# Optimization experiments

Measured on AMD Instinct MI355X. Metric: run time of the kernel, lower is better.

## Reference

```python
import jax, jax.numpy as jnp
import numpy as np
import math

NUM_SOLU, BS, GS, ED, NH = 10, 32, 1000, 128, 8
KD = ED // NH
MSH = 16
NEG = -9e15


def setup_inputs() -> dict:
    key = jax.random.key(0)
    ks = jax.random.split(key, 16)
    node_embed = jax.random.normal(ks[0], (BS, GS, ED), jnp.float32)
    # random TSP tours: permutations per (solution, batch) -> each node a source exactly once
    solutions = jnp.argsort(jax.random.uniform(ks[1], (NUM_SOLU, BS, GS)), axis=-1).astype(jnp.int32)
    costs = jax.random.uniform(ks[2], (NUM_SOLU, BS), minval=1.0, maxval=2.0)  # positive tour costs
    dist = jax.random.uniform(ks[3], (BS, GS, GS), jnp.float32)
    solution_embed_old = jax.random.normal(ks[4], (BS, GS, ED), jnp.float32)
    s = 1.0 / math.sqrt(ED)
    Wq = jax.random.uniform(ks[5], (ED, ED), minval=-s, maxval=s)
    Wk = jax.random.uniform(ks[6], (ED, ED), minval=-s, maxval=s)
    m1 = math.sqrt(0.5)
    m2 = math.sqrt(1.0 / 16.0)
    mix1_weight = jax.random.uniform(ks[7], (NH, 2, MSH), minval=-m1, maxval=m1)
    mix1_bias = jax.random.uniform(ks[8], (NH, MSH), minval=-m1, maxval=m1)
    mix2_weight = jax.random.uniform(ks[9], (NH, MSH, 1), minval=-m2, maxval=m2)
    mix2_bias = jax.random.uniform(ks[10], (NH, 1), minval=-m2, maxval=m2)
    sh = 1.0 / math.sqrt(NH)
    norm_head_w = jax.random.uniform(ks[11], (NH,), minval=-sh, maxval=sh)
    sg = 1.0 / math.sqrt(ED)
    gru_w_ih = jax.random.uniform(ks[12], (3 * ED, ED), minval=-sg, maxval=sg)
    gru_w_hh = jax.random.uniform(ks[13], (3 * ED, ED), minval=-sg, maxval=sg)
    gru_b_ih = jax.random.uniform(ks[14], (3 * ED,), minval=-sg, maxval=sg)
    gru_b_hh = jax.random.uniform(ks[15], (3 * ED,), minval=-sg, maxval=sg)
    return dict(node_embed=node_embed, solutions=solutions, costs=costs, dist=dist,
                solution_embed_old=solution_embed_old, Wq=Wq, Wk=Wk,
                mix1_weight=mix1_weight, mix1_bias=mix1_bias,
                mix2_weight=mix2_weight, mix2_bias=mix2_bias,
                norm_head_w=norm_head_w, gru_w_ih=gru_w_ih, gru_w_hh=gru_w_hh,
                gru_b_ih=gru_b_ih, gru_b_hh=gru_b_hh)


def _forward(node_embed, costs, dist, solution_embed_old, Wq, Wk,
             mix1_weight, mix1_bias, mix2_weight, mix2_bias, norm_head_w,
             gru_w_ih, gru_w_hh, gru_b_ih, gru_b_hh, solutions):
    norm_factor = 1.0 / math.sqrt(KD)
    sqrt_qkv = KD ** 0.5
    nxt = jnp.roll(solutions, -1, axis=-1)                      # [S,B,T] successor in tour
    b_idx = jnp.arange(BS)[None, :, None]
    emb_solu = node_embed[b_idx, solutions]                     # [S,B,T,E] gather
    emb_next = node_embed[b_idx, nxt]                           # [S,B,T,E]
    q = (emb_solu @ Wq.T).reshape(NUM_SOLU, BS, GS, NH, KD)
    k = (emb_next @ Wk.T).reshape(NUM_SOLU, BS, GS, NH, KD)
    dot = jnp.einsum('sbthd,sbthd->sbth', q, k) * (norm_factor / sqrt_qkv)
    edge_cost = dist[b_idx, solutions, nxt]                     # [S,B,T]
    two = jnp.stack([dot, jnp.broadcast_to(edge_cost[..., None], dot.shape)], -1)  # [S,B,T,H,2]
    ms1 = jax.nn.relu(jnp.einsum('sbthe,hem->sbthm', two, mix1_weight) + mix1_bias)
    ms2 = jnp.einsum('sbthm,hmo->sbtho', ms1, mix2_weight)[..., 0] + mix2_bias[:, 0]  # [S,B,T,H]
    e = jnp.einsum('sbth,h->sbt', ms2, norm_head_w)             # norm_head Linear(n_heads,1)
    cost = e / costs[:, :, None]                                # [S,B,T]
    # scatter-add edge scores into dense [B,G,G] attention (tours = permutations,
    # so each (b, src) appears once per solution -> add == per-solution set + sum)
    bb = jnp.broadcast_to(b_idx, solutions.shape)
    attn = jnp.zeros((BS, GS, GS), node_embed.dtype).at[
        bb.reshape(-1), solutions.reshape(-1), nxt.reshape(-1)].add(cost.reshape(-1))
    attn = jnp.where(attn != 0.0, attn, NEG)
    ar = jnp.arange(GS)
    attn = attn.at[:, ar, ar].set(NEG)
    attn = jax.nn.softmax(attn, axis=-1)
    solu_embed = attn @ node_embed                              # [B,G,E]
    # torch GRUCell: gates order r,z,n
    x = solu_embed.reshape(-1, ED)
    h = solution_embed_old.reshape(-1, ED)
    gi = x @ gru_w_ih.T + gru_b_ih
    gh = h @ gru_w_hh.T + gru_b_hh
    i_r, i_z, i_n = jnp.split(gi, 3, axis=-1)
    h_r, h_z, h_n = jnp.split(gh, 3, axis=-1)
    r = jax.nn.sigmoid(i_r + h_r)
    z = jax.nn.sigmoid(i_z + h_z)
    n = jnp.tanh(i_n + r * h_n)
    new = ((1.0 - z) * n + z * h).reshape(BS, GS, ED)
    return jnp.stack([jax.nn.elu(new), new])                    # [2,B,G,E]


def reference(node_embed, solutions, costs, dist, solution_embed_old, Wq, Wk,
              mix1_weight, mix1_bias, mix2_weight, mix2_bias, norm_head_w,
              gru_w_ih, gru_w_hh, gru_b_ih, gru_b_hh):
    out = _forward(node_embed, costs, dist, solution_embed_old, Wq, Wk,
                   mix1_weight, mix1_bias, mix2_weight, mix2_bias, norm_head_w,
                   gru_w_ih, gru_w_hh, gru_b_ih, gru_b_hh, solutions)
    return (out[0], out[1])
```

## Files before the change

kernel.cpp:

```cpp
#include <hip/hip_runtime.h>
#include <math.h>

#define NS 10
#define NB 32
#define NG 1000
#define NE 128
#define NH 8
#define MSH 16

typedef __bf16 bf16x8 __attribute__((ext_vector_type(8)));
typedef float f32x4 __attribute__((ext_vector_type(4)));
typedef unsigned short ushort;
typedef ushort us8 __attribute__((ext_vector_type(8)));

__device__ __forceinline__ ushort f2bf(float f) {
    union { float f; unsigned u; } c; c.f = f;
    unsigned r = c.u + 0x7FFFu + ((c.u >> 16) & 1u);
    return (ushort)(r >> 16);
}
__device__ __forceinline__ float bflo(unsigned u) {
    union { unsigned v; float f; } c; c.v = u << 16; return c.f;
}
__device__ __forceinline__ float bfhi(unsigned u) {
    union { unsigned v; float f; } c; c.v = u & 0xFFFF0000u; return c.f;
}

__global__ __launch_bounds__(512) void qk_prep(
        const float* __restrict__ ne,
        const int* __restrict__ sol, const float* __restrict__ dist,
        const float* __restrict__ Wq, const float* __restrict__ Wk,
        const float* __restrict__ wih, const float* __restrict__ whh,
        float* __restrict__ QKf, ushort* __restrict__ ne_b,
        int* __restrict__ succ, float* __restrict__ edge_val,
        ushort* __restrict__ wih_b, ushort* __restrict__ whh_b) {
    const int tid = threadIdx.x;
    if (blockIdx.x >= 1000) {
        const int bid2 = blockIdx.x - 1000;
        if (bid2 < 625) {
            const int gidx = bid2 * 512 + tid;
            const int sb = gidx / NG;
            const int t = gidx - sb * NG;
            const int* srow = sol + (size_t)sb * NG;
            const int src = srow[t];
            const int tn = (t + 1 == NG) ? 0 : t + 1;
            const int dst = srow[tn];
            const int b = sb & 31;
            succ[(size_t)sb * NG + src] = dst;
            edge_val[(size_t)sb * NG + src] = dist[(size_t)(b * NG + src) * NG + dst];
        } else {
            const int wt = (bid2 - 625) * 512 + tid;
            const int e = wt * 8;
            const float* src = (e < 49152) ? wih : whh;
            ushort* dst = (e < 49152) ? wih_b : whh_b;
            const int off = (e < 49152) ? e : e - 49152;
            const float4 f0 = ((const float4*)(src + off))[0];
            const float4 f1 = ((const float4*)(src + off))[1];
            us8 v;
            v[0] = f2bf(f0.x); v[1] = f2bf(f0.y); v[2] = f2bf(f0.z); v[3] = f2bf(f0.w);
            v[4] = f2bf(f1.x); v[5] = f2bf(f1.y); v[6] = f2bf(f1.z); v[7] = f2bf(f1.w);
            *(us8*)(dst + off) = v;
        }
        return;
    }

    __shared__ __align__(16) ushort A[32 * 128];
    const int rowbase = blockIdx.x * 32;
    {
        const int r = tid >> 4, kc = tid & 15;
        const float4* s4 = (const float4*)(ne + (size_t)(rowbase + r) * NE);
        const float4 f0 = s4[kc * 2], f1 = s4[kc * 2 + 1];
        us8 v;
        v[0] = f2bf(f0.x); v[1] = f2bf(f0.y); v[2] = f2bf(f0.z); v[3] = f2bf(f0.w);
        v[4] = f2bf(f1.x); v[5] = f2bf(f1.y); v[6] = f2bf(f1.z); v[7] = f2bf(f1.w);
        *(us8*)&A[(r * 16 + (kc ^ (r & 7))) * 8] = v;
        *(us8*)&ne_b[(size_t)(rowbase + r) * NE + kc * 8] = v;
    }
    __syncthreads();

    const int w = tid >> 6, l = tid & 63;
    const int lr = l & 15, lg = l >> 4;

    f32x4 acc[2][2] = {};
#pragma unroll
    for (int ks = 0; ks < 4; ++ks) {
        bf16x8 a[2], b[2];
#pragma unroll
        for (int mf = 0; mf < 2; ++mf) {
            const int r = mf * 16 + lr;
            a[mf] = *(const bf16x8*)&A[(r * 16 + ((ks * 4 + lg) ^ (r & 7))) * 8];
        }
#pragma unroll
        for (int nf = 0; nf < 2; ++nf) {
            const int j = w * 32 + nf * 16 + lr;
            const float* Wrow = (j < 128) ? (Wq + (size_t)j * 128 + ks * 32 + lg * 8)
                                          : (Wk + (size_t)(j - 128) * 128 + ks * 32 + lg * 8);
            const float4 wf0 = ((const float4*)Wrow)[0];
            const float4 wf1 = ((const float4*)Wrow)[1];
            union { us8 u; bf16x8 bv; } cv;
            cv.u[0] = f2bf(wf0.x); cv.u[1] = f2bf(wf0.y); cv.u[2] = f2bf(wf0.z); cv.u[3] = f2bf(wf0.w);
            cv.u[4] = f2bf(wf1.x); cv.u[5] = f2bf(wf1.y); cv.u[6] = f2bf(wf1.z); cv.u[7] = f2bf(wf1.w);
            b[nf] = cv.bv;
        }
#pragma unroll
        for (int mf = 0; mf < 2; ++mf)
#pragma unroll
            for (int nf = 0; nf < 2; ++nf)
                acc[mf][nf] = __builtin_amdgcn_mfma_f32_16x16x32_bf16(a[mf], b[nf], acc[mf][nf], 0, 0, 0);
    }
#pragma unroll
    for (int mf = 0; mf < 2; ++mf)
#pragma unroll
        for (int nf = 0; nf < 2; ++nf)
#pragma unroll
            for (int q = 0; q < 4; ++q) {
                const int row = rowbase + mf * 16 + lg * 4 + q;
                const int col = w * 32 + nf * 16 + lr;
                if (w < 4)
                    QKf[(size_t)row * 192 + col] = acc[mf][nf][q];
                else
                    ((ushort*)(QKf + (size_t)row * 192 + 128))[col - 128] = f2bf(acc[mf][nf][q]);
            }
}

__global__ __launch_bounds__(256) void score_agg(
        const int* __restrict__ succ, const float* __restrict__ costs,
        const float* __restrict__ edge_val, const float* __restrict__ QKf,
        const ushort* __restrict__ ne_b,
        const float* __restrict__ m1w, const float* __restrict__ m1b,
        const float* __restrict__ m2w, const float* __restrict__ m2b,
        const float* __restrict__ nhw,
        unsigned* __restrict__ solu_b) {
    __shared__ float w1t[2][MSH][NH];
    __shared__ float b1t[MSH][NH];
    __shared__ float w2t[MSH][NH];
    __shared__ float b2s[NH];
    __shared__ float nws[NH];
    const int tid = threadIdx.x;
    {
        const int h = tid >> 5, e = (tid >> 4) & 1, m = tid & 15;
        w1t[e][m][h] = m1w[tid];
        if (tid < 128) {
            const int h2 = tid >> 4, m2 = tid & 15;
            b1t[m2][h2] = m1b[tid];
            w2t[m2][h2] = m2w[tid];
        }
        if (tid < NH) { b2s[tid] = m2b[tid]; nws[tid] = nhw[tid]; }
    }
    __syncthreads();

    const int bid = blockIdx.x;
    const int xcd = bid & 7;
    const int idx = bid >> 3;
    const int b = xcd + 8 * (idx / 250);
    const int g = (idx % 250) * 4 + (tid >> 6);
    const int lane = tid & 63;
    const int w = b * NG + g;
    const int h = lane & 7;
    const int sg = lane >> 3;

    int dstp[2]; float edgep[2];
    {
        const size_t o0 = (size_t)(sg * NB + b) * NG + g;
        const size_t o1 = (size_t)((8 + sg) * NB + b) * NG + g;
        dstp[0] = succ[o0];
        dstp[1] = (sg < 2) ? succ[o1] : 0;
        edgep[0] = edge_val[o0];
        edgep[1] = (sg < 2) ? edge_val[o1] : 0.f;
    }

    int d[NS];
#pragma unroll
    for (int s = 0; s < 8; ++s) d[s] = __shfl(dstp[0], s * 8);
    d[8] = __shfl(dstp[1], 0); d[9] = __shfl(dstp[1], 8);

    unsigned urow[NS];
#pragma unroll
    for (int s = 0; s < NS; ++s)
        urow[s] = ((const unsigned*)(ne_b + (size_t)(b * NG + d[s]) * NE))[lane];

    const float4* Qf = (const float4*)(QKf + (size_t)w * 192) + h * 4;
    const float4 qa = Qf[0], qb = Qf[1], qc = Qf[2], qd = Qf[3];
    uint4 k0p[2], k1p[2];
#pragma unroll
    for (int pass = 0; pass < 2; ++pass) {
        const uint4* Kr = (const uint4*)(QKf + (size_t)(b * NG + dstp[pass]) * 192 + 128);
        k0p[pass] = Kr[h * 2]; k1p[pass] = Kr[h * 2 + 1];
    }

    float val_p[2];
#pragma unroll
    for (int pass = 0; pass < 2; ++pass) {
        const uint4 k0 = k0p[pass], k1 = k1p[pass];
        float dd = qa.x * bflo(k0.x) + qa.y * bfhi(k0.x)
                 + qa.z * bflo(k0.y) + qa.w * bfhi(k0.y)
                 + qb.x * bflo(k0.z) + qb.y * bfhi(k0.z)
                 + qb.z * bflo(k0.w) + qb.w * bfhi(k0.w)
                 + qc.x * bflo(k1.x) + qc.y * bfhi(k1.x)
                 + qc.z * bflo(k1.y) + qc.w * bfhi(k1.y)
                 + qd.x * bflo(k1.z) + qd.y * bfhi(k1.z)
                 + qd.z * bflo(k1.w) + qd.w * bfhi(k1.w);
        dd *= 0.0625f;
        float ms2 = b2s[h];
#pragma unroll
        for (int m = 0; m < MSH; ++m) {
            float t = dd * w1t[0][m][h] + edgep[pass] * w1t[1][m][h] + b1t[m][h];
            t = fmaxf(t, 0.f);
            ms2 += t * w2t[m][h];
        }
        float contrib = ms2 * nws[h];
        contrib += __shfl_xor(contrib, 1);
        contrib += __shfl_xor(contrib, 2);
        contrib += __shfl_xor(contrib, 4);
        val_p[pass] = contrib;
    }

    const float va = __shfl(val_p[0], (lane & 7) * 8);
    const float vb = __shfl(val_p[1], (lane & 1) * 8);
    const int   da = __shfl(dstp[0], (lane & 7) * 8);
    const int   db = __shfl(dstp[1], (lane & 1) * 8);
    float v_own = (lane < 8) ? va : vb;
    const int d_own = (lane < 8) ? da : db;
    const int cidx = (lane < NS) ? lane : 0;
    v_own *= __builtin_amdgcn_rcpf(costs[cidx * NB + b]);

    float acc = v_own;
    bool first = true;
#pragma unroll
    for (int p = 0; p < NS; ++p) {
        const int   d_p = __shfl(d_own, p);
        const float v_p = __shfl(v_own, p);
        const bool eq = (d_p == d_own);
        first = first && (!eq || p >= lane);
        acc += (eq && p > lane) ? v_p : 0.f;
    }
    const bool surv = (lane < NS) && first && (acc != 0.f);

    float mval = surv ? acc : -3.0e38f;
    mval = fmaxf(mval, __shfl_xor(mval, 1));
    mval = fmaxf(mval, __shfl_xor(mval, 2));
    mval = fmaxf(mval, __shfl_xor(mval, 4));
    mval = fmaxf(mval, __shfl_xor(mval, 8));
    const float e = surv ? __expf(acc - mval) : 0.f;
    float den = e;
    den += __shfl_xor(den, 1);
    den += __shfl_xor(den, 2);
    den += __shfl_xor(den, 4);
    den += __shfl_xor(den, 8);
    const float wt_own = e * __builtin_amdgcn_rcpf(den);

    const bool any = (__ballot(surv) != 0ull);

    float a0 = 0.f, a1 = 0.f;
    if (!any) {
        const unsigned* base = (const unsigned*)(ne_b + (size_t)b * NG * NE);
        for (int n = 0; n < NG; ++n) {
            const unsigned u = base[n * 64 + lane];
            a0 += bflo(u); a1 += bfhi(u);
        }
        const float invG = 1.f / NG;
        a0 *= invG; a1 *= invG;
    } else {
#pragma unroll
        for (int s = 0; s < NS; ++s) {
            const float wt = __shfl(wt_own, s);
            a0 += wt * bflo(urow[s]);
            a1 += wt * bfhi(urow[s]);
        }
    }
    solu_b[(size_t)w * 64 + lane] = (unsigned)f2bf(a0) | ((unsigned)f2bf(a1) << 16);
}

__global__ __launch_bounds__(512) void gru_mfma(
        const ushort* __restrict__ x_b,
        const float* __restrict__ h_in,
        const ushort* __restrict__ wih_b, const ushort* __restrict__ whh_b,
        const float* __restrict__ bih, const float* __restrict__ bhh,
        float* __restrict__ out0, float* __restrict__ out1) {
    __shared__ __align__(16) ushort X[32 * 128];
    __shared__ __align__(16) ushort H[32 * 128];
    const int tid = threadIdx.x;
    const int rowbase = blockIdx.x * 32;

    {
        const int r = tid >> 4, kc = tid & 15;
        us8 xv = *(const us8*)&x_b[(size_t)(rowbase + r) * NE + kc * 8];
        *(us8*)&X[(r * 16 + (kc ^ (r & 7))) * 8] = xv;
        const float4* h4 = (const float4*)(h_in + (size_t)(rowbase + r) * NE);
        const float4 f0 = h4[kc * 2], f1 = h4[kc * 2 + 1];
        us8 hv;
        hv[0] = f2bf(f0.x); hv[1] = f2bf(f0.y); hv[2] = f2bf(f0.z); hv[3] = f2bf(f0.w);
        hv[4] = f2bf(f1.x); hv[5] = f2bf(f1.y); hv[6] = f2bf(f1.z); hv[7] = f2bf(f1.w);
        *(us8*)&H[(r * 16 + (kc ^ (r & 7))) * 8] = hv;
    }
    __syncthreads();

    const int w = tid >> 6, l = tid & 63;
    const int lr = l & 15, lg = l >> 4;
    const int j = w * 16 + lr;

    f32x4 acc[2][6] = {};
#pragma unroll
    for (int ks = 0; ks < 4; ++ks) {
        bf16x8 ax[2], ah[2], bb[6];
#pragma unroll
        for (int mf = 0; mf < 2; ++mf) {
            const int r = mf * 16 + lr;
            const int c = (r * 16 + ((ks * 4 + lg) ^ (r & 7))) * 8;
            ax[mf] = *(const bf16x8*)&X[c];
            ah[mf] = *(const bf16x8*)&H[c];
        }
#pragma unroll
        for (int g = 0; g < 3; ++g) {
            bb[g]     = *(const bf16x8*)&wih_b[(size_t)(g * 128 + j) * 128 + ks * 32 + lg * 8];
            bb[g + 3] = *(const bf16x8*)&whh_b[(size_t)(g * 128 + j) * 128 + ks * 32 + lg * 8];
        }
#pragma unroll
        for (int mf = 0; mf < 2; ++mf) {
#pragma unroll
            for (int g = 0; g < 3; ++g) {
                acc[mf][g]     = __builtin_amdgcn_mfma_f32_16x16x32_bf16(ax[mf], bb[g],     acc[mf][g],     0, 0, 0);
                acc[mf][g + 3] = __builtin_amdgcn_mfma_f32_16x16x32_bf16(ah[mf], bb[g + 3], acc[mf][g + 3], 0, 0, 0);
            }
        }
    }

    const float bi0 = bih[j], bi1 = bih[128 + j], bi2 = bih[256 + j];
    const float bh0 = bhh[j], bh1 = bhh[128 + j], bh2 = bhh[256 + j];
#pragma unroll
    for (int mf = 0; mf < 2; ++mf) {
#pragma unroll
        for (int q = 0; q < 4; ++q) {
            const int row = rowbase + mf * 16 + lg * 4 + q;
            const float ir = acc[mf][0][q] + bi0;
            const float iz = acc[mf][1][q] + bi1;
            const float in_ = acc[mf][2][q] + bi2;
            const float hr = acc[mf][3][q] + bh0;
            const float hz = acc[mf][4][q] + bh1;
            const float hn = acc[mf][5][q] + bh2;
            const float rr = 1.f / (1.f + expf(-(ir + hr)));
            const float zz = 1.f / (1.f + expf(-(iz + hz)));
            const float nn = tanhf(in_ + rr * hn);
            const float hv = h_in[(size_t)row * NE + j];
            const float nv = (1.f - zz) * nn + zz * hv;
            const size_t o = (size_t)row * NE + j;
            out1[o] = nv;
            out0[o] = (nv > 0.f) ? nv : expm1f(nv);
        }
    }
}

extern "C" void kernel_launch(void* const* d_in, const int* in_sizes, int n_in,
                              void* d_out, int out_size, void* d_ws, size_t ws_size,
                              hipStream_t stream) {
    const float* ne    = (const float*)d_in[0];
    const int*   sol   = (const int*)d_in[1];
    const float* costs = (const float*)d_in[2];
    const float* dist  = (const float*)d_in[3];
    const float* old_h = (const float*)d_in[4];
    const float* Wq    = (const float*)d_in[5];
    const float* Wk    = (const float*)d_in[6];
    const float* m1w   = (const float*)d_in[7];
    const float* m1b   = (const float*)d_in[8];
    const float* m2w   = (const float*)d_in[9];
    const float* m2b   = (const float*)d_in[10];
    const float* nhw   = (const float*)d_in[11];
    const float* wih   = (const float*)d_in[12];
    const float* whh   = (const float*)d_in[13];
    const float* bih   = (const float*)d_in[14];
    const float* bhh   = (const float*)d_in[15];

    float* out0 = (float*)d_out;
    float* out1 = out0 + (size_t)NB * NG * NE;

    float*    QKf      = (float*)d_ws;
    ushort*   ne_b     = (ushort*)(QKf + (size_t)NB * NG * 192);
    int*      succ     = (int*)(ne_b + (size_t)NB * NG * NE);
    float*    edge_val = (float*)(succ + (size_t)NS * NB * NG);
    unsigned* solu_b   = (unsigned*)(edge_val + (size_t)NS * NB * NG);
    ushort*   wih_b    = (ushort*)(solu_b + (size_t)NB * NG * 64);
    ushort*   whh_b    = wih_b + 384 * 128;

    qk_prep<<<1000 + 625 + 24, 512, 0, stream>>>(
        ne, sol, dist, Wq, Wk, wih, whh,
        QKf, ne_b, succ, edge_val, wih_b, whh_b);
    score_agg<<<(NB * NG * 64) / 256, 256, 0, stream>>>(
        succ, costs, edge_val, QKf, ne_b, m1w, m1b, m2w, m2b, nhw, solu_b);
    gru_mfma<<<(NB * NG) / 32, 512, 0, stream>>>(
        (const ushort*)solu_b, old_h, wih_b, whh_b, bih, bhh, out0, out1);
}
```

Measured before the change: 101.5 us.

## Store Q in bf16 and process two nodes per wave in score_agg

Measured after the change: 98.74 us. 2.7% less time.

```diff
diff --git a/kernel.cpp b/kernel.cpp
--- a/kernel.cpp
+++ b/kernel.cpp
@@ -24,13 +24,19 @@
 __device__ __forceinline__ float bfhi(unsigned u) {
     union { unsigned v; float f; } c; c.v = u & 0xFFFF0000u; return c.f;
 }
+__device__ __forceinline__ float dot8(uint4 q, uint4 k) {
+    return bflo(q.x) * bflo(k.x) + bfhi(q.x) * bfhi(k.x)
+         + bflo(q.y) * bflo(k.y) + bfhi(q.y) * bfhi(k.y)
+         + bflo(q.z) * bflo(k.z) + bfhi(q.z) * bfhi(k.z)
+         + bflo(q.w) * bflo(k.w) + bfhi(q.w) * bfhi(k.w);
+}
 
 __global__ __launch_bounds__(512) void qk_prep(
         const float* __restrict__ ne,
         const int* __restrict__ sol, const float* __restrict__ dist,
         const float* __restrict__ Wq, const float* __restrict__ Wk,
         const float* __restrict__ wih, const float* __restrict__ whh,
-        float* __restrict__ QKf, ushort* __restrict__ ne_b,
+        ushort* __restrict__ QKb, ushort* __restrict__ ne_b,
         int* __restrict__ succ, float* __restrict__ edge_val,
         ushort* __restrict__ wih_b, ushort* __restrict__ whh_b) {
     const int tid = threadIdx.x;
@@ -115,16 +121,13 @@
             for (int q = 0; q < 4; ++q) {
                 const int row = rowbase + mf * 16 + lg * 4 + q;
                 const int col = w * 32 + nf * 16 + lr;
-                if (w < 4)
-                    QKf[(size_t)row * 192 + col] = acc[mf][nf][q];
-                else
-                    ((ushort*)(QKf + (size_t)row * 192 + 128))[col - 128] = f2bf(acc[mf][nf][q]);
+                QKb[(size_t)row * 256 + col] = f2bf(acc[mf][nf][q]);
             }
 }
 
 __global__ __launch_bounds__(256) void score_agg(
         const int* __restrict__ succ, const float* __restrict__ costs,
-        const float* __restrict__ edge_val, const float* __restrict__ QKf,
+        const float* __restrict__ edge_val, const ushort* __restrict__ QKb,
         const ushort* __restrict__ ne_b,
         const float* __restrict__ m1w, const float* __restrict__ m1b,
         const float* __restrict__ m2w, const float* __restrict__ m2b,
@@ -151,123 +154,131 @@
     const int bid = blockIdx.x;
     const int xcd = bid & 7;
     const int idx = bid >> 3;
-    const int b = xcd + 8 * (idx / 250);
-    const int g = (idx % 250) * 4 + (tid >> 6);
+    const int b = xcd + 8 * (idx / 125);
+    const int gbase = (idx % 125) * 8 + ((tid >> 6) << 1);
     const int lane = tid & 63;
-    const int w = b * NG + g;
     const int h = lane & 7;
     const int sg = lane >> 3;
 
-    int dstp[2]; float edgep[2];
-    {
-        const size_t o0 = (size_t)(sg * NB + b) * NG + g;
-        const size_t o1 = (size_t)((8 + sg) * NB + b) * NG + g;
-        dstp[0] = succ[o0];
-        dstp[1] = (sg < 2) ? succ[o1] : 0;
-        edgep[0] = edge_val[o0];
-        edgep[1] = (sg < 2) ? edge_val[o1] : 0.f;
-    }
-
-    int d[NS];
-#pragma unroll
-    for (int s = 0; s < 8; ++s) d[s] = __shfl(dstp[0], s * 8);
-    d[8] = __shfl(dstp[1], 0); d[9] = __shfl(dstp[1], 8);
-
-    unsigned urow[NS];
-#pragma unroll
-    for (int s = 0; s < NS; ++s)
-        urow[s] = ((const unsigned*)(ne_b + (size_t)(b * NG + d[s]) * NE))[lane];
-
-    const float4* Qf = (const float4*)(QKf + (size_t)w * 192) + h * 4;
-    const float4 qa = Qf[0], qb = Qf[1], qc = Qf[2], qd = Qf[3];
-    uint4 k0p[2], k1p[2];
-#pragma unroll
-    for (int pass = 0; pass < 2; ++pass) {
-        const uint4* Kr = (const uint4*)(QKf + (size_t)(b * NG + dstp[pass]) * 192 + 128);
-        k0p[pass] = Kr[h * 2]; k1p[pass] = Kr[h * 2 + 1];
-    }
-
-    float val_p[2];
-#pragma unroll
-    for (int pass = 0; pass < 2; ++pass) {
-        const uint4 k0 = k0p[pass], k1 = k1p[pass];
-        float dd = qa.x * bflo(k0.x) + qa.y * bfhi(k0.x)
-                 + qa.z * bflo(k0.y) + qa.w * bfhi(k0.y)
-                 + qb.x * bflo(k0.z) + qb.y * bfhi(k0.z)
-                 + qb.z * bflo(k0.w) + qb.w * bfhi(k0.w)
-                 + qc.x * bflo(k1.x) + qc.y * bfhi(k1.x)
-                 + qc.z * bflo(k1.y) + qc.w * bfhi(k1.y)
-                 + qd.x * bflo(k1.z) + qd.y * bfhi(k1.z)
-                 + qd.z * bflo(k1.w) + qd.w * bfhi(k1.w);
-        dd *= 0.0625f;
-        float ms2 = b2s[h];
-#pragma unroll
-        for (int m = 0; m < MSH; ++m) {
-            float t = dd * w1t[0][m][h] + edgep[pass] * w1t[1][m][h] + b1t[m][h];
-            t = fmaxf(t, 0.f);
-            ms2 += t * w2t[m][h];
-        }
-        float contrib = ms2 * nws[h];
-        contrib += __shfl_xor(contrib, 1);
-        contrib += __shfl_xor(contrib, 2);
-        contrib += __shfl_xor(contrib, 4);
-        val_p[pass] = contrib;
-    }
-
-    const float va = __shfl(val_p[0], (lane & 7) * 8);
-    const float vb = __shfl(val_p[1], (lane & 1) * 8);
-    const int   da = __shfl(dstp[0], (lane & 7) * 8);
-    const int   db = __shfl(dstp[1], (lane & 1) * 8);
-    float v_own = (lane < 8) ? va : vb;
-    const int d_own = (lane < 8) ? da : db;
-    const int cidx = (lane < NS) ? lane : 0;
-    v_own *= __builtin_amdgcn_rcpf(costs[cidx * NB + b]);
-
-    float acc = v_own;
-    bool first = true;
-#pragma unroll
-    for (int p = 0; p < NS; ++p) {
-        const int   d_p = __shfl(d_own, p);
-        const float v_p = __shfl(v_own, p);
-        const bool eq = (d_p == d_own);
-        first = first && (!eq || p >= lane);
-        acc += (eq && p > lane) ? v_p : 0.f;
-    }
-    const bool surv = (lane < NS) && first && (acc != 0.f);
-
-    float mval = surv ? acc : -3.0e38f;
-    mval = fmaxf(mval, __shfl_xor(mval, 1));
-    mval = fmaxf(mval, __shfl_xor(mval, 2));
-    mval = fmaxf(mval, __shfl_xor(mval, 4));
-    mval = fmaxf(mval, __shfl_xor(mval, 8));
-    const float e = surv ? __expf(acc - mval) : 0.f;
-    float den = e;
-    den += __shfl_xor(den, 1);
-    den += __shfl_xor(den, 2);
-    den += __shfl_xor(den, 4);
-    den += __shfl_xor(den, 8);
-    const float wt_own = e * __builtin_amdgcn_rcpf(den);
-
-    const bool any = (__ballot(surv) != 0ull);
-
-    float a0 = 0.f, a1 = 0.f;
-    if (!any) {
-        const unsigned* base = (const unsigned*)(ne_b + (size_t)b * NG * NE);
-        for (int n = 0; n < NG; ++n) {
-            const unsigned u = base[n * 64 + lane];
-            a0 += bflo(u); a1 += bfhi(u);
-        }
-        const float invG = 1.f / NG;
-        a0 *= invG; a1 *= invG;
-    } else {
-#pragma unroll
-        for (int s = 0; s < NS; ++s) {
-            const float wt = __shfl(wt_own, s);
-            a0 += wt * bflo(urow[s]);
-            a1 += wt * bfhi(urow[s]);
-        }
-    }
-    solu_b[(size_t)w * 64 + lane] = (unsigned)f2bf(a0) | ((unsigned)f2bf(a1) << 16);
+    int dstp[2][2]; float edgep[2][2];
+#pragma unroll
+    for (int r = 0; r < 2; ++r) {
+        const size_t o0 = (size_t)(sg * NB + b) * NG + (gbase + r);
+        const size_t o1 = (size_t)((8 + sg) * NB + b) * NG + (gbase + r);
+        dstp[r][0] = succ[o0];
+        dstp[r][1] = (sg < 2) ? succ[o1] : 0;
+        edgep[r][0] = edge_val[o0];
+        edgep[r][1] = (sg < 2) ? edge_val[o1] : 0.f;
+    }
+
+    uint4 kk[2][2][2];
+#pragma unroll
+    for (int r = 0; r < 2; ++r)
+#pragma unroll
+        for (int p = 0; p < 2; ++p) {
+            const uint4* Kr = (const uint4*)(QKb + (size_t)(b * NG + dstp[r][p]) * 256 + 128);
+            kk[r][p][0] = Kr[h * 2]; kk[r][p][1] = Kr[h * 2 + 1];
+        }
+
+    uint4 qq[2][2];
+#pragma unroll
+    for (int r = 0; r < 2; ++r) {
+        const uint4* Qr = (const uint4*)(QKb + (size_t)(b * NG + gbase + r) * 256);
+        qq[r][0] = Qr[h * 2]; qq[r][1] = Qr[h * 2 + 1];
+    }
+
+    unsigned urow[2][NS];
+#pragma unroll
+    for (int r = 0; r < 2; ++r) {
+        int dd;
+#pragma unroll
+        for (int s = 0; s < 8; ++s) {
+            dd = __shfl(dstp[r][0], s * 8);
+            urow[r][s] = ((const unsigned*)(ne_b + (size_t)(b * NG + dd) * NE))[lane];
+        }
+        dd = __shfl(dstp[r][1], 0);
+        urow[r][8] = ((const unsigned*)(ne_b + (size_t)(b * NG + dd) * NE))[lane];
+        dd = __shfl(dstp[r][1], 8);
+        urow[r][9] = ((const unsigned*)(ne_b + (size_t)(b * NG + dd) * NE))[lane];
+    }
+
+    float val_p[2][2];
+#pragma unroll
+    for (int r = 0; r < 2; ++r)
+#pragma unroll
+        for (int p = 0; p < 2; ++p) {
+            float dd = (dot8(qq[r][0], kk[r][p][0]) + dot8(qq[r][1], kk[r][p][1])) * 0.0625f;
+            float ms2 = b2s[h];
+#pragma unroll
+            for (int m = 0; m < MSH; ++m) {
+                float t = fmaf(dd, w1t[0][m][h], fmaf(edgep[r][p], w1t[1][m][h], b1t[m][h]));
+                t = fmaxf(t, 0.f);
+                ms2 = fmaf(t, w2t[m][h], ms2);
+            }
+            float contrib = ms2 * nws[h];
+            contrib += __shfl_xor(contrib, 1);
+            contrib += __shfl_xor(contrib, 2);
+            contrib += __shfl_xor(contrib, 4);
+            val_p[r][p] = contrib;
+        }
+
+    const float cinv = __builtin_amdgcn_rcpf(costs[((lane < NS) ? lane : 0) * NB + b]);
+#pragma unroll
+    for (int r = 0; r < 2; ++r) {
+        const float va = __shfl(val_p[r][0], (lane & 7) * 8);
+        const float vb = __shfl(val_p[r][1], (lane & 1) * 8);
+        const int   da = __shfl(dstp[r][0], (lane & 7) * 8);
+        const int   db = __shfl(dstp[r][1], (lane & 1) * 8);
+        float v_own = ((lane < 8) ? va : vb) * cinv;
+        const int d_own = (lane < 8) ? da : db;
+
+        float acc = v_own;
+        bool first = true;
+#pragma unroll
+        for (int p = 0; p < NS; ++p) {
+            const int   d_p = __shfl(d_own, p);
+            const float v_p = __shfl(v_own, p);
+            const bool eq = (d_p == d_own);
+            first = first && (!eq || p >= lane);
+            acc += (eq && p > lane) ? v_p : 0.f;
+        }
+        const bool surv = (lane < NS) && first && (acc != 0.f);
+
+        float mval = surv ? acc : -3.0e38f;
+        mval = fmaxf(mval, __shfl_xor(mval, 1));
+        mval = fmaxf(mval, __shfl_xor(mval, 2));
+        mval = fmaxf(mval, __shfl_xor(mval, 4));
+        mval = fmaxf(mval, __shfl_xor(mval, 8));
+        const float e = surv ? __expf(acc - mval) : 0.f;
+        float den = e;
+        den += __shfl_xor(den, 1);
+        den += __shfl_xor(den, 2);
+        den += __shfl_xor(den, 4);
+        den += __shfl_xor(den, 8);
+        const float wt_own = e * __builtin_amdgcn_rcpf(den);
+
+        const bool any = (__ballot(surv) != 0ull);
+
+        float a0 = 0.f, a1 = 0.f;
+        if (!any) {
+            const unsigned* base = (const unsigned*)(ne_b + (size_t)b * NG * NE);
+            for (int n = 0; n < NG; ++n) {
+                const unsigned u = base[n * 64 + lane];
+                a0 += bflo(u); a1 += bfhi(u);
+            }
+            const float invG = 1.f / NG;
+            a0 *= invG; a1 *= invG;
+        } else {
+#pragma unroll
+            for (int s = 0; s < NS; ++s) {
+                const float wt = __shfl(wt_own, s);
+                a0 += wt * bflo(urow[r][s]);
+                a1 += wt * bfhi(urow[r][s]);
+            }
+        }
+        solu_b[(size_t)(b * NG + gbase + r) * 64 + lane] =
+            (unsigned)f2bf(a0) | ((unsigned)f2bf(a1) << 16);
+    }
 }
 
 __global__ __launch_bounds__(512) void gru_mfma(
@@ -372,8 +383,8 @@
     float* out0 = (float*)d_out;
     float* out1 = out0 + (size_t)NB * NG * NE;
 
-    float*    QKf      = (float*)d_ws;
-    ushort*   ne_b     = (ushort*)(QKf + (size_t)NB * NG * 192);
+    ushort*   QKb      = (ushort*)d_ws;
+    ushort*   ne_b     = QKb + (size_t)NB * NG * 256;
     int*      succ     = (int*)(ne_b + (size_t)NB * NG * NE);
     float*    edge_val = (float*)(succ + (size_t)NS * NB * NG);
     unsigned* solu_b   = (unsigned*)(edge_val + (size_t)NS * NB * NG);
@@ -382,9 +393,9 @@
 
     qk_prep<<<1000 + 625 + 24, 512, 0, stream>>>(
         ne, sol, dist, Wq, Wk, wih, whh,
-        QKf, ne_b, succ, edge_val, wih_b, whh_b);
-    score_agg<<<(NB * NG * 64) / 256, 256, 0, stream>>>(
-        succ, costs, edge_val, QKf, ne_b, m1w, m1b, m2w, m2b, nhw, solu_b);
+        QKb, ne_b, succ, edge_val, wih_b, whh_b);
+    score_agg<<<4000, 256, 0, stream>>>(
+        succ, costs, edge_val, QKb, ne_b, m1w, m1b, m2w, m2b, nhw, solu_b);
     gru_mfma<<<(NB * NG) / 32, 512, 0, stream>>>(
         (const ushort*)solu_b, old_h, wih_b, whh_b, bih, bhh, out0, out1);
 }
```
